# Optimization experiments

Measured on AMD Instinct MI355X. Metric: run time of the kernel, lower is better.

Reference implementation:

```python
import jax, jax.numpy as jnp
import numpy as np

B, T, C = 2, 2048, 2048
N_HEAD, N_KV_HEAD = 16, 4
HEAD_DIM = C // N_HEAD          # 128
N_REP = N_HEAD // N_KV_HEAD     # 4
HALF = HEAD_DIM // 2            # 64


def setup_inputs() -> dict:
    key = jax.random.key(0)
    ks = jax.random.split(key, 6)
    x = jax.random.normal(ks[0], (B, T, C), dtype=jnp.float32)
    # real RoPE tables: theta_i = 10000^{-2i/d}, angles = t * theta_i
    inv_freq = 1.0 / (10000.0 ** (jnp.arange(0, HALF, dtype=jnp.float32) / HALF))
    angles = jnp.arange(T, dtype=jnp.float32)[:, None] * inv_freq[None, :]  # (T, HALF)
    freqs_cos = jnp.cos(angles)
    freqs_sin = jnp.sin(angles)
    s = 0.02
    wq = jax.random.normal(ks[1], (C, C), dtype=jnp.float32) * s
    wk = jax.random.normal(ks[2], (N_KV_HEAD * HEAD_DIM, C), dtype=jnp.float32) * s
    wv = jax.random.normal(ks[3], (N_KV_HEAD * HEAD_DIM, C), dtype=jnp.float32) * s
    wo = jax.random.normal(ks[4], (C, C), dtype=jnp.float32) * s
    return {"x": x, "freqs_cos": freqs_cos, "freqs_sin": freqs_sin,
            "wq": wq, "wk": wk, "wv": wv, "wo": wo}


def _apply_rope(t, cos, sin):
    # t: (B, T, H, D); rotate consecutive pairs (llama view_as_complex layout)
    te = t[..., 0::2]   # (B, T, H, D/2)
    to = t[..., 1::2]
    c = cos[None, :, None, :]
    s = sin[None, :, None, :]
    oe = te * c - to * s
    oo = te * s + to * c
    return jnp.stack([oe, oo], axis=-1).reshape(t.shape)


def reference(x, freqs_cos, freqs_sin, wq, wk, wv, wo):
    Bx, Tx, Cx = x.shape
    q = (x @ wq.T).reshape(Bx, Tx, N_HEAD, HEAD_DIM)
    k = (x @ wk.T).reshape(Bx, Tx, N_KV_HEAD, HEAD_DIM)
    v = (x @ wv.T).reshape(Bx, Tx, N_KV_HEAD, HEAD_DIM)
    q = _apply_rope(q, freqs_cos, freqs_sin)
    k = _apply_rope(k, freqs_cos, freqs_sin)
    # GQA: group query heads by kv head instead of repeat_interleave'ing KV
    qg = q.reshape(Bx, Tx, N_KV_HEAD, N_REP, HEAD_DIM)
    scale = 1.0 / jnp.sqrt(jnp.asarray(HEAD_DIM, dtype=q.dtype))
    # scores: (B, kv_head, rep, T, T)
    scores = jnp.einsum('btgrd,bsgd->bgrts', qg, k) * scale
    causal = jnp.tril(jnp.ones((Tx, Tx), dtype=bool))
    scores = jnp.where(causal[None, None, None], scores, jnp.asarray(-1e30, dtype=scores.dtype))
    probs = jax.nn.softmax(scores, axis=-1)
    y = jnp.einsum('bgrts,bsgd->btgrd', probs, v).reshape(Bx, Tx, Cx)
    return y @ wo.T
```

## Files before the change

kernel.cpp:

```cpp
#include <hip/hip_runtime.h>

#define T_SEQ 2048
#define NB    2
#define NHEAD 16
#define NKV   4
#define HD    128
#define CDIM  2048
#define QKV_W 3072
#define MROWS 4096

#define QSCALE 0.12752648137154393f

typedef unsigned int  uint;
typedef unsigned short ushort;

typedef __attribute__((ext_vector_type(8))) __bf16 bf16x8;
typedef __attribute__((ext_vector_type(4))) float  floatx4;

#if __has_builtin(__builtin_amdgcn_exp2f)
#define EXP2F(x) __builtin_amdgcn_exp2f(x)
#else
#define EXP2F(x) exp2f(x)
#endif

__device__ __forceinline__ uint bf16rne(float f) {
  uint u = __float_as_uint(f);
  u += 0x7fffu + ((u >> 16) & 1u);
  return u >> 16;
}
__device__ __forceinline__ float bflo(uint w) { return __uint_as_float(w << 16); }
__device__ __forceinline__ float bfhi(uint w) { return __uint_as_float(w & 0xffff0000u); }

__device__ __forceinline__ void block_bar() {
  __builtin_amdgcn_sched_barrier(0);
  __builtin_amdgcn_s_barrier();
  __builtin_amdgcn_sched_barrier(0);
}

__global__ void cast_f32_bf16x2(const float* __restrict__ in, uint* __restrict__ out, int n2) {
  int i = blockIdx.x * 256 + threadIdx.x;
  if (i < n2) {
    float2 v = ((const float2*)in)[i];
    out[i] = bf16rne(v.x) | (bf16rne(v.y) << 16);
  }
}

__device__ __forceinline__ void store_elem(ushort* C, size_t idx, float v) { C[idx] = (ushort)bf16rne(v); }
__device__ __forceinline__ void store_elem(float*  C, size_t idx, float v) { C[idx] = v; }

template <typename OutT>
__global__ __launch_bounds__(256, 2) void gemm_bt(const ushort* __restrict__ A,
                                                  const ushort* __restrict__ Bt,
                                                  OutT* __restrict__ C,
                                                  int M, int N, int K,
                                                  int vcol0, ushort* __restrict__ vt) {
  __shared__ ushort smem[32768];
  const int tid  = threadIdx.x;
  const int wave = tid >> 6, lane = tid & 63;
  const int quad = lane >> 4, l16 = lane & 15;
  const int wm = wave >> 1, wn = wave & 1;
  const int mBase = blockIdx.y << 7;
  const int nBase = blockIdx.x << 7;
  const int NKT = K >> 6;

  floatx4 acc[4][4];
#pragma unroll
  for (int i = 0; i < 4; ++i)
#pragma unroll
    for (int j = 0; j < 4; ++j)
#pragma unroll
      for (int r = 0; r < 4; ++r) acc[i][j][r] = 0.f;

  const int srow = tid >> 3;
  const int sc8  = ((tid & 7) ^ (srow & 7)) << 3;
  const ushort* gA = A  + (size_t)(mBase + srow) * K + sc8;
  const ushort* gB = Bt + (size_t)(nBase + srow) * K + sc8;
  ushort* ldsA = smem + (wave << 9);
  ushort* ldsB = smem + 16384 + (wave << 9);

#define STAGE(k0, bsel)                                                               \
  do {                                                                                \
    _Pragma("unroll")                                                                 \
    for (int it_ = 0; it_ < 4; ++it_)                                                 \
      __builtin_amdgcn_global_load_lds(                                               \
          (const __attribute__((address_space(1))) void*)(gA + (size_t)it_ * 32 * K + (k0)), \
          (__attribute__((address_space(3))) void*)(ldsA + (bsel) + it_ * 2048), 16, 0, 0);  \
    _Pragma("unroll")                                                                 \
    for (int it_ = 0; it_ < 4; ++it_)                                                 \
      __builtin_amdgcn_global_load_lds(                                               \
          (const __attribute__((address_space(1))) void*)(gB + (size_t)it_ * 32 * K + (k0)), \
          (__attribute__((address_space(3))) void*)(ldsB + (bsel) + it_ * 2048), 16, 0, 0);  \
  } while (0)

  const int aro = ((wm << 6) + l16) * 64;
  const int bro = 16384 + ((wn << 6) + l16) * 64;
  const int sw0 = ((quad       ^ (l16 & 7)) << 3);
  const int sw1 = (((quad + 4) ^ (l16 & 7)) << 3);

  STAGE(0, 0);
  STAGE(64, 8192);
  asm volatile("s_waitcnt vmcnt(8)" ::: "memory");
  block_bar();

  for (int t = 0; t < NKT; ++t) {
    const int bsel = (t & 1) << 13;
#pragma unroll
    for (int kk = 0; kk < 2; ++kk) {
      const int sw = kk ? sw1 : sw0;
      bf16x8 bfrag[4];
#pragma unroll
      for (int j = 0; j < 4; ++j)
        bfrag[j] = *(const bf16x8*)&smem[bro + bsel + j * 1024 + sw];
#pragma unroll
      for (int i = 0; i < 4; ++i) {
        bf16x8 ai = *(const bf16x8*)&smem[aro + bsel + i * 1024 + sw];
#pragma unroll
        for (int j = 0; j < 4; ++j)
          acc[i][j] = __builtin_amdgcn_mfma_f32_16x16x32_bf16(ai, bfrag[j], acc[i][j], 0, 0, 0);
      }
    }
    asm volatile("s_waitcnt lgkmcnt(0)" ::: "memory");
    block_bar();
    if (t + 2 < NKT) {
      STAGE((t + 2) << 6, bsel);
      asm volatile("s_waitcnt vmcnt(8)" ::: "memory");
      block_bar();
    } else if (t + 1 < NKT) {
      asm volatile("s_waitcnt vmcnt(0)" ::: "memory");
      block_bar();
    }
  }
#undef STAGE

#pragma unroll
  for (int i = 0; i < 4; ++i) {
    const int rowb = mBase + (wm << 6) + (i << 4) + (quad << 2);
#pragma unroll
    for (int j = 0; j < 4; ++j) {
      const int colb = nBase + (wn << 6) + (j << 4);
      const int col  = colb + l16;
      if (colb < vcol0) {
#pragma unroll
        for (int r = 0; r < 4; ++r)
          store_elem(C, (size_t)(rowb + r) * N + col, acc[i][j][r]);
      } else {
        const int vcol = col - vcol0;
        const int bb = rowb >> 11;
        const int t  = rowb & 2047;
        uint2 pw;
        pw.x = bf16rne(acc[i][j][0]) | (bf16rne(acc[i][j][1]) << 16);
        pw.y = bf16rne(acc[i][j][2]) | (bf16rne(acc[i][j][3]) << 16);
        *(uint2*)(vt + (((size_t)(bb << 9) + vcol) << 11) + t) = pw;
      }
    }
  }
}

__global__ void rope_kernel(ushort* __restrict__ qkv, const float* __restrict__ fc,
                            const float* __restrict__ fs) {
  int idx  = blockIdx.x * 256 + threadIdx.x;
  int d2   = idx & 63;
  int rest = idx >> 6;
  int hh   = rest % 20;
  int bt   = rest / 20;
  int t    = bt & (T_SEQ - 1);
  float c = fc[(t << 6) + d2];
  float s = fs[(t << 6) + d2];
  int col = (hh < 16) ? ((hh << 7) + (d2 << 1)) : (2048 + ((hh - 16) << 7) + (d2 << 1));
  float m = (hh < 16) ? QSCALE : 1.0f;
  uint* p = (uint*)(qkv + (size_t)bt * QKV_W + col);
  uint w = *p;
  float e = bflo(w), o = bfhi(w);
  float oe = (e * c - o * s) * m;
  float oo = (e * s + o * c) * m;
  *p = bf16rne(oe) | (bf16rne(oo) << 16);
}

__global__ __launch_bounds__(512, 2) void attn_mfma(const ushort* __restrict__ qkv,
                                                    const ushort* __restrict__ vtg,
                                                    ushort* __restrict__ y) {
  __shared__ ushort smem[51456];
  ushort* sP = smem + 32768;
  float*  sOf = (float*)smem;
  ushort* sO  = smem + 33792;
  float*  sLf = (float*)(smem + 51200);

  const int tid  = threadIdx.x;
  const int wave = tid >> 6, lane = tid & 63;
  const int quad = lane >> 4, l16 = lane & 15;
  const int w_s = wave & 1;
  const int w_t = wave >> 1;
  const int h = blockIdx.y, b = blockIdx.z, kh = h >> 2;
  const size_t bT = (size_t)b * T_SEQ;

  union { uint4 u; bf16x8 v; } ones_u;
  ones_u.u = make_uint4(0x3F803F80u, 0x3F803F80u, 0x3F803F80u, 0x3F803F80u);
  const bf16x8 onesf = ones_u.v;

  const int kr  = tid >> 4;
  const int kc8 = tid & 15;
  const ushort* gK = qkv + (bT + kr) * QKV_W + 2048 + kh * HD + ((kc8 ^ (kr & 7)) << 3);
  const int vd  = tid >> 3;
  const int vsc = tid & 7;
  const ushort* gV = vtg + (((size_t)(b << 9) + (kh << 7) + vd) << 11) + ((vsc ^ (vd & 7)) << 3);

#define STAGE_ATTN(cn, bo_)                                                            \
  do {                                                                                 \
    _Pragma("unroll")                                                                  \
    for (int it_ = 0; it_ < 2; ++it_)                                                  \
      __builtin_amdgcn_global_load_lds(                                                \
          (const __attribute__((address_space(1))) void*)(gK + ((size_t)(cn) * 64 + it_ * 32) * QKV_W), \
          (__attribute__((address_space(3))) void*)(smem + (bo_) + (wave << 9) + it_ * 4096), 16, 0, 0); \
    _Pragma("unroll")                                                                  \
    for (int it_ = 0; it_ < 2; ++it_)                                                  \
      __builtin_amdgcn_global_load_lds(                                                \
          (const __attribute__((address_space(1))) void*)(gV + ((size_t)it_ << 17) + (cn) * 64), \
          (__attribute__((address_space(3))) void*)(smem + 16384 + (bo_) + (wave << 9) + it_ * 4096), 16, 0, 0); \
  } while (0)

  for (int half = 0; half < 2; ++half) {
    const int xt = half ? (15 - (int)blockIdx.x) : (int)blockIdx.x;
    const int t0 = xt << 7;
    const int sblk = w_s << 5, tblk = w_t << 5;

    bf16x8 qf[2][4];
#pragma unroll
    for (int tt = 0; tt < 2; ++tt)
#pragma unroll
      for (int kk = 0; kk < 4; ++kk)
        qf[tt][kk] = *(const bf16x8*)(qkv + (bT + t0 + tblk + tt * 16 + l16) * QKV_W +
                                      h * HD + kk * 32 + quad * 8);

    floatx4 oacc[2][8];
    floatx4 lacc[2];
#pragma unroll
    for (int tt = 0; tt < 2; ++tt) {
#pragma unroll
      for (int r = 0; r < 4; ++r) lacc[tt][r] = 0.f;
#pragma unroll
      for (int dt = 0; dt < 8; ++dt)
#pragma unroll
        for (int r = 0; r < 4; ++r) oacc[tt][dt][r] = 0.f;
    }

    const int nch = (t0 >> 6) + 2;

    STAGE_ATTN(0, 0);

    for (int ch = 0; ch < nch; ++ch) {
      __syncthreads();
      if (ch + 1 < nch) STAGE_ATTN(ch + 1, ((ch + 1) & 1) << 13);
      const int bo = (ch & 1) << 13;
      const int s0 = ch << 6;

      const bool fullmask = (s0 + sblk) > (t0 + tblk + 31);
      if (!fullmask) {
        floatx4 accS[2][2];
#pragma unroll
        for (int st = 0; st < 2; ++st)
#pragma unroll
          for (int tt = 0; tt < 2; ++tt)
#pragma unroll
            for (int r = 0; r < 4; ++r) accS[st][tt][r] = 0.f;

#pragma unroll
        for (int kk = 0; kk < 4; ++kk) {
          bf16x8 kf0 = *(const bf16x8*)(smem + bo + (sblk + l16) * 128 +
                                        ((((kk << 2) + quad) ^ (l16 & 7)) << 3));
          bf16x8 kf1 = *(const bf16x8*)(smem + bo + (sblk + 16 + l16) * 128 +
                                        ((((kk << 2) + quad) ^ (l16 & 7)) << 3));
#pragma unroll
          for (int tt = 0; tt < 2; ++tt)
            accS[0][tt] = __builtin_amdgcn_mfma_f32_16x16x32_bf16(kf0, qf[tt][kk], accS[0][tt], 0, 0, 0);
#pragma unroll
          for (int tt = 0; tt < 2; ++tt)
            accS[1][tt] = __builtin_amdgcn_mfma_f32_16x16x32_bf16(kf1, qf[tt][kk], accS[1][tt], 0, 0, 0);
        }

        const bool diag = (s0 + sblk + 31) > (t0 + tblk);
#pragma unroll
        for (int st = 0; st < 2; ++st)
#pragma unroll
          for (int tt = 0; tt < 2; ++tt) {
            float p[4];
            if (diag) {
              const int sg = s0 + sblk + st * 16 + quad * 4;
              const int tg = t0 + tblk + tt * 16 + l16;
#pragma unroll
              for (int r = 0; r < 4; ++r)
                p[r] = (sg + r <= tg) ? EXP2F(accS[st][tt][r]) : 0.f;
            } else {
#pragma unroll
              for (int r = 0; r < 4; ++r) p[r] = EXP2F(accS[st][tt][r]);
            }
            uint2 pw;
            pw.x = (__float_as_uint(p[0]) >> 16) | (__float_as_uint(p[1]) & 0xFFFF0000u);
            pw.y = (__float_as_uint(p[2]) >> 16) | (__float_as_uint(p[3]) & 0xFFFF0000u);
            *(uint2*)(sP + (tblk + tt * 16 + l16) * 72 + sblk + st * 16 + quad * 4) = pw;
          }

        bf16x8 pf[2];
#pragma unroll
        for (int tt = 0; tt < 2; ++tt) {
          pf[tt] = *(const bf16x8*)(sP + (tblk + tt * 16 + l16) * 72 + sblk + (quad << 3));
          lacc[tt] = __builtin_amdgcn_mfma_f32_16x16x32_bf16(pf[tt], onesf, lacc[tt], 0, 0, 0);
        }
#pragma unroll
        for (int dt = 0; dt < 8; ++dt) {
          bf16x8 vf = *(const bf16x8*)(smem + 16384 + bo + (dt * 16 + l16) * 64 +
                                       ((((w_s << 2) + quad) ^ (l16 & 7)) << 3));
#pragma unroll
          for (int tt = 0; tt < 2; ++tt)
            oacc[tt][dt] = __builtin_amdgcn_mfma_f32_16x16x32_bf16(pf[tt], vf, oacc[tt][dt], 0, 0, 0);
        }
      }
    }

    __syncthreads();
    if (w_s == 0) {
#pragma unroll
      for (int tt = 0; tt < 2; ++tt) {
#pragma unroll
        for (int dt = 0; dt < 8; ++dt)
#pragma unroll
          for (int r = 0; r < 4; ++r)
            sOf[(tblk + tt * 16 + quad * 4 + r) * 132 + dt * 16 + l16] = oacc[tt][dt][r];
        if (l16 == 0) {
#pragma unroll
          for (int r = 0; r < 4; ++r)
            sLf[tblk + tt * 16 + quad * 4 + r] = lacc[tt][r];
        }
      }
    }
    __syncthreads();
    if (w_s == 1) {
#pragma unroll
      for (int tt = 0; tt < 2; ++tt) {
        float linv[4];
#pragma unroll
        for (int r = 0; r < 4; ++r)
          linv[r] = 1.0f / (sLf[tblk + tt * 16 + quad * 4 + r] + lacc[tt][r]);
#pragma unroll
        for (int dt = 0; dt < 8; ++dt)
#pragma unroll
          for (int r = 0; r < 4; ++r) {
            float v = (sOf[(tblk + tt * 16 + quad * 4 + r) * 132 + dt * 16 + l16] +
                       oacc[tt][dt][r]) * linv[r];
            sO[(tblk + tt * 16 + quad * 4 + r) * 136 + dt * 16 + l16] = (ushort)bf16rne(v);
          }
      }
    }
    __syncthreads();
#pragma unroll
    for (int it = 0; it < 4; ++it) {
      int idx = it * 512 + tid;
      int rr = idx >> 4, c8 = idx & 15;
      *(uint4*)(y + (bT + t0 + rr) * CDIM + h * HD + c8 * 8) =
          *(const uint4*)(sO + rr * 136 + c8 * 8);
    }
  }
#undef STAGE_ATTN
}

extern "C" void kernel_launch(void* const* d_in, const int* in_sizes, int n_in,
                              void* d_out, int out_size, void* d_ws, size_t ws_size,
                              hipStream_t stream) {
  const float* x    = (const float*)d_in[0];
  const float* fcos = (const float*)d_in[1];
  const float* fsin = (const float*)d_in[2];
  const float* wq   = (const float*)d_in[3];
  const float* wk   = (const float*)d_in[4];
  const float* wv   = (const float*)d_in[5];
  const float* wo   = (const float*)d_in[6];
  float* out = (float*)d_out;

  ushort* ws    = (ushort*)d_ws;
  ushort* xb    = ws;
  ushort* yb    = ws;
  ushort* wqkvb = ws    + 8388608;
  ushort* wob   = wqkvb + 6291456;
  ushort* qkv   = wob   + 4194304;
  ushort* vtg   = qkv   + 12582912;

  cast_f32_bf16x2<<<16384, 256, 0, stream>>>(x,  (uint*)xb,    4194304);
  cast_f32_bf16x2<<< 8192, 256, 0, stream>>>(wq, (uint*)wqkvb, 2097152);
  cast_f32_bf16x2<<< 2048, 256, 0, stream>>>(wk, (uint*)(wqkvb + 4194304), 524288);
  cast_f32_bf16x2<<< 2048, 256, 0, stream>>>(wv, (uint*)(wqkvb + 5242880), 524288);
  cast_f32_bf16x2<<< 8192, 256, 0, stream>>>(wo, (uint*)wob,   2097152);

  gemm_bt<ushort><<<dim3(QKV_W / 128, MROWS / 128), 256, 0, stream>>>(
      xb, wqkvb, qkv, MROWS, QKV_W, CDIM, 2560, vtg);

  rope_kernel<<<20480, 256, 0, stream>>>(qkv, fcos, fsin);

  attn_mfma<<<dim3(8, NHEAD, NB), 512, 0, stream>>>(qkv, vtg, yb);

  gemm_bt<float><<<dim3(CDIM / 128, MROWS / 128), 256, 0, stream>>>(
      yb, wob, out, MROWS, CDIM, CDIM, 1 << 30, nullptr);
}
```

Baseline: 284.6 us.

## Widen GEMM tiles to 128x256 with 8 waves and triple-buffered LDS pipeline

The bt-GEMM now runs 512 threads per block on a 128x256 output tile, laid out as 2x4 waves. It keeps three LDS stages (144 KB) and interleaves the global-to-LDS loads for stage t+2 between the two k-halves of MFMA work, with s_setprio raised around the MFMA bursts. The goal is more reuse per tile and better overlap of loads with compute. In exchange there is one block per CU, fewer blocks in the grid (96 and 128 for the two GEMMs), and more register and LDS pressure.

```diff
diff --git a/kernel.cpp b/kernel.cpp
--- a/kernel.cpp
+++ b/kernel.cpp
@@ -49,18 +49,18 @@
 __device__ __forceinline__ void store_elem(float*  C, size_t idx, float v) { C[idx] = v; }
 
 template <typename OutT>
-__global__ __launch_bounds__(256, 2) void gemm_bt(const ushort* __restrict__ A,
+__global__ __launch_bounds__(512, 1) void gemm_bt(const ushort* __restrict__ A,
                                                   const ushort* __restrict__ Bt,
                                                   OutT* __restrict__ C,
                                                   int M, int N, int K,
                                                   int vcol0, ushort* __restrict__ vt) {
-  __shared__ ushort smem[32768];
+  __shared__ ushort smem[73728];
   const int tid  = threadIdx.x;
   const int wave = tid >> 6, lane = tid & 63;
   const int quad = lane >> 4, l16 = lane & 15;
-  const int wm = wave >> 1, wn = wave & 1;
+  const int wm = wave >> 2, wn = wave & 3;
   const int mBase = blockIdx.y << 7;
-  const int nBase = blockIdx.x << 7;
+  const int nBase = blockIdx.x << 8;
   const int NKT = K >> 6;
 
   floatx4 acc[4][4];
@@ -73,64 +73,101 @@
 
   const int srow = tid >> 3;
   const int sc8  = ((tid & 7) ^ (srow & 7)) << 3;
-  const ushort* gA = A  + (size_t)(mBase + srow) * K + sc8;
-  const ushort* gB = Bt + (size_t)(nBase + srow) * K + sc8;
-  ushort* ldsA = smem + (wave << 9);
-  ushort* ldsB = smem + 16384 + (wave << 9);
-
-#define STAGE(k0, bsel)                                                               \
-  do {                                                                                \
-    _Pragma("unroll")                                                                 \
-    for (int it_ = 0; it_ < 4; ++it_)                                                 \
-      __builtin_amdgcn_global_load_lds(                                               \
-          (const __attribute__((address_space(1))) void*)(gA + (size_t)it_ * 32 * K + (k0)), \
-          (__attribute__((address_space(3))) void*)(ldsA + (bsel) + it_ * 2048), 16, 0, 0);  \
-    _Pragma("unroll")                                                                 \
-    for (int it_ = 0; it_ < 4; ++it_)                                                 \
-      __builtin_amdgcn_global_load_lds(                                               \
-          (const __attribute__((address_space(1))) void*)(gB + (size_t)it_ * 32 * K + (k0)), \
-          (__attribute__((address_space(3))) void*)(ldsB + (bsel) + it_ * 2048), 16, 0, 0);  \
-  } while (0)
-
-  const int aro = ((wm << 6) + l16) * 64;
-  const int bro = 16384 + ((wn << 6) + l16) * 64;
-  const int sw0 = ((quad       ^ (l16 & 7)) << 3);
-  const int sw1 = (((quad + 4) ^ (l16 & 7)) << 3);
-
-  STAGE(0, 0);
-  STAGE(64, 8192);
-  asm volatile("s_waitcnt vmcnt(8)" ::: "memory");
+  const ushort* gAa = A  + (size_t)(mBase + srow) * K + sc8;
+  const ushort* gBa = Bt + (size_t)(nBase + srow) * K + sc8;
+
+#define GLL(gptr, loff)                                                              \
+  __builtin_amdgcn_global_load_lds((const __attribute__((address_space(1))) void*)(gptr), \
+      (__attribute__((address_space(3))) void*)(smem + (loff) + (wave << 9)), 16, 0, 0)
+
+  {
+    GLL(gAa,                    0);
+    GLL(gAa + (size_t)64 * K,   4096);
+    GLL(gBa,                    24576);
+    GLL(gBa + (size_t)64 * K,   24576 + 4096);
+    GLL(gBa + (size_t)128 * K,  24576 + 8192);
+    GLL(gBa + (size_t)192 * K,  24576 + 12288);
+    GLL(gAa + 64,                   8192);
+    GLL(gAa + (size_t)64 * K + 64,  8192 + 4096);
+    GLL(gBa + 64,                   40960);
+    GLL(gBa + (size_t)64 * K + 64,  40960 + 4096);
+    GLL(gBa + (size_t)128 * K + 64, 40960 + 8192);
+    GLL(gBa + (size_t)192 * K + 64, 40960 + 12288);
+  }
+  asm volatile("s_waitcnt vmcnt(6)" ::: "memory");
   block_bar();
 
+  int cur = 0;
   for (int t = 0; t < NKT; ++t) {
-    const int bsel = (t & 1) << 13;
-#pragma unroll
-    for (int kk = 0; kk < 2; ++kk) {
-      const int sw = kk ? sw1 : sw0;
-      bf16x8 bfrag[4];
+    const int curA = cur * 8192;
+    const int curB = 24576 + cur * 16384;
+    const int tgt  = (cur == 0) ? 2 : cur - 1;
+    const int tgtA = tgt * 8192;
+    const int tgtB = 24576 + tgt * 16384;
+    const int k2   = (t + 2) << 6;
+    const bool stg = (t + 2 < NKT);
+
+    {
+      const int sw = ((quad ^ (l16 & 7)) << 3);
+      bf16x8 af[4], bfr[4];
+#pragma unroll
+      for (int i = 0; i < 4; ++i)
+        af[i]  = *(const bf16x8*)&smem[curA + ((wm << 6) + (i << 4) + l16) * 64 + sw];
 #pragma unroll
       for (int j = 0; j < 4; ++j)
-        bfrag[j] = *(const bf16x8*)&smem[bro + bsel + j * 1024 + sw];
-#pragma unroll
-      for (int i = 0; i < 4; ++i) {
-        bf16x8 ai = *(const bf16x8*)&smem[aro + bsel + i * 1024 + sw];
+        bfr[j] = *(const bf16x8*)&smem[curB + ((wn << 6) + (j << 4) + l16) * 64 + sw];
+      if (stg) {
+        GLL(gAa + k2,                  tgtA);
+        GLL(gAa + (size_t)64 * K + k2, tgtA + 4096);
+        GLL(gBa + k2,                  tgtB);
+      }
+      block_bar();
+      asm volatile("s_waitcnt lgkmcnt(0)" ::: "memory");
+      __builtin_amdgcn_sched_barrier(0);
+      __builtin_amdgcn_s_setprio(1);
+#pragma unroll
+      for (int i = 0; i < 4; ++i)
 #pragma unroll
         for (int j = 0; j < 4; ++j)
-          acc[i][j] = __builtin_amdgcn_mfma_f32_16x16x32_bf16(ai, bfrag[j], acc[i][j], 0, 0, 0);
-      }
-    }
-    asm volatile("s_waitcnt lgkmcnt(0)" ::: "memory");
-    block_bar();
-    if (t + 2 < NKT) {
-      STAGE((t + 2) << 6, bsel);
-      asm volatile("s_waitcnt vmcnt(8)" ::: "memory");
+          acc[i][j] = __builtin_amdgcn_mfma_f32_16x16x32_bf16(af[i], bfr[j], acc[i][j], 0, 0, 0);
+      __builtin_amdgcn_s_setprio(0);
       block_bar();
-    } else if (t + 1 < NKT) {
-      asm volatile("s_waitcnt vmcnt(0)" ::: "memory");
+    }
+
+    {
+      const int sw = (((quad + 4) ^ (l16 & 7)) << 3);
+      bf16x8 af[4], bfr[4];
+#pragma unroll
+      for (int i = 0; i < 4; ++i)
+        af[i]  = *(const bf16x8*)&smem[curA + ((wm << 6) + (i << 4) + l16) * 64 + sw];
+#pragma unroll
+      for (int j = 0; j < 4; ++j)
+        bfr[j] = *(const bf16x8*)&smem[curB + ((wn << 6) + (j << 4) + l16) * 64 + sw];
+      if (stg) {
+        GLL(gBa + (size_t)64 * K + k2,  tgtB + 4096);
+        GLL(gBa + (size_t)128 * K + k2, tgtB + 8192);
+        GLL(gBa + (size_t)192 * K + k2, tgtB + 12288);
+      }
       block_bar();
-    }
+      asm volatile("s_waitcnt lgkmcnt(0)" ::: "memory");
+      __builtin_amdgcn_sched_barrier(0);
+      __builtin_amdgcn_s_setprio(1);
+#pragma unroll
+      for (int i = 0; i < 4; ++i)
+#pragma unroll
+        for (int j = 0; j < 4; ++j)
+          acc[i][j] = __builtin_amdgcn_mfma_f32_16x16x32_bf16(af[i], bfr[j], acc[i][j], 0, 0, 0);
+      __builtin_amdgcn_s_setprio(0);
+      if (t + 2 < NKT) {
+        asm volatile("s_waitcnt vmcnt(6)" ::: "memory");
+      } else if (t + 1 < NKT) {
+        asm volatile("s_waitcnt vmcnt(0)" ::: "memory");
+      }
+      block_bar();
+    }
+    cur = (cur == 2) ? 0 : cur + 1;
   }
-#undef STAGE
+#undef GLL
 
 #pragma unroll
   for (int i = 0; i < 4; ++i) {
@@ -388,13 +425,13 @@
   cast_f32_bf16x2<<< 2048, 256, 0, stream>>>(wv, (uint*)(wqkvb + 5242880), 524288);
   cast_f32_bf16x2<<< 8192, 256, 0, stream>>>(wo, (uint*)wob,   2097152);
 
-  gemm_bt<ushort><<<dim3(QKV_W / 128, MROWS / 128), 256, 0, stream>>>(
+  gemm_bt<ushort><<<dim3(QKV_W / 256, MROWS / 128), 512, 0, stream>>>(
       xb, wqkvb, qkv, MROWS, QKV_W, CDIM, 2560, vtg);
 
   rope_kernel<<<20480, 256, 0, stream>>>(qkv, fcos, fsin);
 
   attn_mfma<<<dim3(8, NHEAD, NB), 512, 0, stream>>>(qkv, vtg, yb);
 
-  gemm_bt<float><<<dim3(CDIM / 128, MROWS / 128), 256, 0, stream>>>(
+  gemm_bt<float><<<dim3(CDIM / 256, MROWS / 128), 512, 0, stream>>>(
       yb, wob, out, MROWS, CDIM, CDIM, 1 << 30, nullptr);
 }
```

Measured after the change: 300.0 us. 5.4% more time.

## Fuse RoPE into QKV GEMM epilogue and merge weight casts into one kernel

Applied to the files above, without the earlier changes.

The RoPE rotation and Q scaling move into the QKV GEMM epilogue. Each lane swaps with its neighbour column via a shuffle to form the even/odd pair and reads the cos/sin tables directly. This removes a separate read-modify-write pass over the Q/K part of the qkv buffer and one launch. The five separate cast launches become a single kernel that picks its source by index range, saving launch overhead. In exchange, the epilogue does scalar bf16 stores with per-row table loads.

```diff
diff --git a/kernel.cpp b/kernel.cpp
--- a/kernel.cpp
+++ b/kernel.cpp
@@ -37,23 +37,31 @@
   __builtin_amdgcn_sched_barrier(0);
 }
 
-__global__ void cast_f32_bf16x2(const float* __restrict__ in, uint* __restrict__ out, int n2) {
+__global__ void cast_all(const float* __restrict__ x,  const float* __restrict__ wq,
+                         const float* __restrict__ wk, const float* __restrict__ wv,
+                         const float* __restrict__ wo, uint* __restrict__ out) {
   int i = blockIdx.x * 256 + threadIdx.x;
-  if (i < n2) {
-    float2 v = ((const float2*)in)[i];
-    out[i] = bf16rne(v.x) | (bf16rne(v.y) << 16);
-  }
+  const float2* src; int off;
+  if (i < 4194304)      { src = (const float2*)x;  off = 0; }
+  else if (i < 6291456) { src = (const float2*)wq; off = 4194304; }
+  else if (i < 6815744) { src = (const float2*)wk; off = 6291456; }
+  else if (i < 7340032) { src = (const float2*)wv; off = 6815744; }
+  else                  { src = (const float2*)wo; off = 7340032; }
+  float2 v = src[i - off];
+  out[i] = bf16rne(v.x) | (bf16rne(v.y) << 16);
 }
 
 __device__ __forceinline__ void store_elem(ushort* C, size_t idx, float v) { C[idx] = (ushort)bf16rne(v); }
 __device__ __forceinline__ void store_elem(float*  C, size_t idx, float v) { C[idx] = v; }
 
-template <typename OutT>
+template <typename OutT, bool ROPE>
 __global__ __launch_bounds__(256, 2) void gemm_bt(const ushort* __restrict__ A,
                                                   const ushort* __restrict__ Bt,
                                                   OutT* __restrict__ C,
                                                   int M, int N, int K,
-                                                  int vcol0, ushort* __restrict__ vt) {
+                                                  int vcol0, ushort* __restrict__ vt,
+                                                  const float* __restrict__ fc,
+                                                  const float* __restrict__ fs) {
   __shared__ ushort smem[32768];
   const int tid  = threadIdx.x;
   const int wave = tid >> 6, lane = tid & 63;
@@ -140,9 +148,27 @@
       const int colb = nBase + (wn << 6) + (j << 4);
       const int col  = colb + l16;
       if (colb < vcol0) {
-#pragma unroll
-        for (int r = 0; r < 4; ++r)
-          store_elem(C, (size_t)(rowb + r) * N + col, acc[i][j][r]);
+        if constexpr (ROPE) {
+          const float m  = (colb < 2048) ? QSCALE : 1.0f;
+          const int  d2  = ((colb & 127) + l16) >> 1;
+          const bool odd = (l16 & 1);
+#pragma unroll
+          for (int r = 0; r < 4; ++r) {
+            const int trow = (rowb + r) & (T_SEQ - 1);
+            float c = fc[(trow << 6) + d2];
+            float s = fs[(trow << 6) + d2];
+            float v = acc[i][j][r];
+            float p = __shfl_xor(v, 1);
+            float e = odd ? p : v;
+            float o = odd ? v : p;
+            float outv = (odd ? (e * s + o * c) : (e * c - o * s)) * m;
+            C[(size_t)(rowb + r) * N + col] = (ushort)bf16rne(outv);
+          }
+        } else {
+#pragma unroll
+          for (int r = 0; r < 4; ++r)
+            store_elem(C, (size_t)(rowb + r) * N + col, acc[i][j][r]);
+        }
       } else {
         const int vcol = col - vcol0;
         const int bb = rowb >> 11;
@@ -154,26 +180,6 @@
       }
     }
   }
-}
-
-__global__ void rope_kernel(ushort* __restrict__ qkv, const float* __restrict__ fc,
-                            const float* __restrict__ fs) {
-  int idx  = blockIdx.x * 256 + threadIdx.x;
-  int d2   = idx & 63;
-  int rest = idx >> 6;
-  int hh   = rest % 20;
-  int bt   = rest / 20;
-  int t    = bt & (T_SEQ - 1);
-  float c = fc[(t << 6) + d2];
-  float s = fs[(t << 6) + d2];
-  int col = (hh < 16) ? ((hh << 7) + (d2 << 1)) : (2048 + ((hh - 16) << 7) + (d2 << 1));
-  float m = (hh < 16) ? QSCALE : 1.0f;
-  uint* p = (uint*)(qkv + (size_t)bt * QKV_W + col);
-  uint w = *p;
-  float e = bflo(w), o = bfhi(w);
-  float oe = (e * c - o * s) * m;
-  float oo = (e * s + o * c) * m;
-  *p = bf16rne(oe) | (bf16rne(oo) << 16);
 }
 
 __global__ __launch_bounds__(512, 2) void attn_mfma(const ushort* __restrict__ qkv,
@@ -382,19 +388,13 @@
   ushort* qkv   = wob   + 4194304;
   ushort* vtg   = qkv   + 12582912;
 
-  cast_f32_bf16x2<<<16384, 256, 0, stream>>>(x,  (uint*)xb,    4194304);
-  cast_f32_bf16x2<<< 8192, 256, 0, stream>>>(wq, (uint*)wqkvb, 2097152);
-  cast_f32_bf16x2<<< 2048, 256, 0, stream>>>(wk, (uint*)(wqkvb + 4194304), 524288);
-  cast_f32_bf16x2<<< 2048, 256, 0, stream>>>(wv, (uint*)(wqkvb + 5242880), 524288);
-  cast_f32_bf16x2<<< 8192, 256, 0, stream>>>(wo, (uint*)wob,   2097152);
-
-  gemm_bt<ushort><<<dim3(QKV_W / 128, MROWS / 128), 256, 0, stream>>>(
-      xb, wqkvb, qkv, MROWS, QKV_W, CDIM, 2560, vtg);
-
-  rope_kernel<<<20480, 256, 0, stream>>>(qkv, fcos, fsin);
+  cast_all<<<36864, 256, 0, stream>>>(x, wq, wk, wv, wo, (uint*)ws);
+
+  gemm_bt<ushort, true><<<dim3(QKV_W / 128, MROWS / 128), 256, 0, stream>>>(
+      xb, wqkvb, qkv, MROWS, QKV_W, CDIM, 2560, vtg, fcos, fsin);
 
   attn_mfma<<<dim3(8, NHEAD, NB), 512, 0, stream>>>(qkv, vtg, yb);
 
-  gemm_bt<float><<<dim3(CDIM / 128, MROWS / 128), 256, 0, stream>>>(
-      yb, wob, out, MROWS, CDIM, CDIM, 1 << 30, nullptr);
-}
+  gemm_bt<float, false><<<dim3(CDIM / 128, MROWS / 128), 256, 0, stream>>>(
+      yb, wob, out, MROWS, CDIM, CDIM, 1 << 30, nullptr, nullptr, nullptr);
+}
```

Result: no change. 281.7 us (-1.0%).
